# Optimization experiments

Hardware: AMD Instinct MI355X
Metric: run time of the kernel (lower is better)

Reference implementation:

```python
import jax, jax.numpy as jnp
import numpy as np

TYPE_N = 5
EPS = 1e-6  # torch F.pairwise_distance default eps, added to the difference before the norm


def setup_inputs() -> dict:
    key = jax.random.key(0)
    k1, k2 = jax.random.split(key)
    N, D = 200000, 256
    x = jax.random.normal(k1, (N, D), dtype=jnp.float32)
    y_real = jax.random.normal(k2, (N, TYPE_N), dtype=jnp.float32)
    return {"x": x, "y_real": y_real}


def reference(x, y_real):
    xf = x.reshape(x.shape[0], -1)                      # [N, D]
    labels = jnp.argmax(y_real, axis=1)                 # [N]
    dt = xf.dtype

    # per-class counts and centroid sums (segment reduce, one pass)
    counts = jax.ops.segment_sum(jnp.ones((xf.shape[0],), dt), labels, num_segments=TYPE_N)  # [C]
    sums = jax.ops.segment_sum(xf, labels, num_segments=TYPE_N)                              # [C, D]
    safe_counts = jnp.maximum(counts, 1.0)
    center = jnp.where(counts[:, None] > 0, sums / safe_counts[:, None], 0.0)                # [C, D]

    # positive loss: mean intra-class distance to centroid, summed over present classes
    d = jnp.linalg.norm(xf - center[labels] + EPS, axis=1)                                   # [N]
    per_class_mean = jax.ops.segment_sum(d, labels, num_segments=TYPE_N) / safe_counts       # [C]
    present = (counts > 0) & (jnp.sum(center, axis=1) != 0)                                  # [C]
    loss_pos = jnp.sum(jnp.where(present, per_class_mean, 0.0))
    real_n = jnp.sum(present.astype(dt))

    # negative loss: mean pairwise distance between present centers (C is tiny)
    diff = center[:, None, :] - center[None, :, :] + EPS                                     # [C, C, D]
    pd = jnp.linalg.norm(diff, axis=-1)                                                      # [C, C]
    triu = jnp.triu(jnp.ones((TYPE_N, TYPE_N), bool), k=1)
    pair_mask = triu & present[:, None] & present[None, :]
    n_pairs = real_n * (real_n - 1.0) / 2.0
    loss_neg = jnp.where(real_n > 1,
                         jnp.sum(jnp.where(pair_mask, pd, 0.0)) / jnp.maximum(n_pairs, 1.0),
                         0.0)

    loss_pos = jnp.where(real_n > 0, loss_pos / jnp.maximum(real_n, 1.0), 1.0)
    return loss_pos / (loss_neg + loss_pos)
```

## Files before the change

### kernel.cpp

```cpp
#include <hip/hip_runtime.h>
#include <math.h>

#define TYPE_N 5
#define D 256
#define EPS 1e-6f
#define NCOPY 16
#define RPB 100

#define OFF_CNTP   (NCOPY * TYPE_N * D)
#define OFF_CENTER (OFF_CNTP + NCOPY * TYPE_N)
#define OFF_CNTF   (OFF_CENTER + TYPE_N * D)
#define OFF_DSUM   (OFF_CNTF + TYPE_N)
#define OFF_CME    (OFF_DSUM + NCOPY * TYPE_N)
#define WS_FLOATS  (OFF_CME + TYPE_N * D)

__device__ __forceinline__ int argmax5(const float* __restrict__ yr) {
    int lab = 0;
    float best = yr[0];
    #pragma unroll
    for (int c = 1; c < TYPE_N; ++c) {
        float v = yr[c];
        if (v > best) { best = v; lab = c; }
    }
    return lab;
}

__global__ __launch_bounds__(256) void k1_sums(const float* __restrict__ x,
                                               const float* __restrict__ y,
                                               float* __restrict__ ws, int N) {
    __shared__ float lsum[4][TYPE_N][D];
    __shared__ float lcnt[4][TYPE_N];
    const int lane = threadIdx.x & 63;
    const int sub  = threadIdx.x >> 6;
    const int r0   = blockIdx.x * RPB;
    const int rows = (N - r0 < RPB) ? (N - r0) : RPB;

    float acc[TYPE_N][4] = {};
    float cnt[TYPE_N] = {};
    const float cw = (lane == 0) ? 1.0f : 0.0f;

    const int ng = rows >> 2;
    for (int i = 0; i < ng; ++i) {
        const int rb = r0 + i * 4;
        const int lab0 = argmax5(y + (size_t)rb * TYPE_N);
        const int lab1 = argmax5(y + (size_t)(rb + 1) * TYPE_N);
        const int lab2 = argmax5(y + (size_t)(rb + 2) * TYPE_N);
        const int lab3 = argmax5(y + (size_t)(rb + 3) * TYPE_N);
        int lab = lab0;
        lab = (sub == 1) ? lab1 : lab;
        lab = (sub == 2) ? lab2 : lab;
        lab = (sub == 3) ? lab3 : lab;
        const float4 v = *reinterpret_cast<const float4*>(
            x + (size_t)(rb + sub) * D + lane * 4);
        #pragma unroll
        for (int c = 0; c < TYPE_N; ++c) {
            const float m = (lab == c) ? 1.0f : 0.0f;
            acc[c][0] = fmaf(m, v.x, acc[c][0]);
            acc[c][1] = fmaf(m, v.y, acc[c][1]);
            acc[c][2] = fmaf(m, v.z, acc[c][2]);
            acc[c][3] = fmaf(m, v.w, acc[c][3]);
            cnt[c]    = fmaf(m, cw, cnt[c]);
        }
    }
    for (int r = r0 + (ng << 2) + sub; r < r0 + rows; r += 4) {
        const int lab = argmax5(y + (size_t)r * TYPE_N);
        const float4 v = *reinterpret_cast<const float4*>(
            x + (size_t)r * D + lane * 4);
        #pragma unroll
        for (int c = 0; c < TYPE_N; ++c) {
            const float m = (lab == c) ? 1.0f : 0.0f;
            acc[c][0] = fmaf(m, v.x, acc[c][0]);
            acc[c][1] = fmaf(m, v.y, acc[c][1]);
            acc[c][2] = fmaf(m, v.z, acc[c][2]);
            acc[c][3] = fmaf(m, v.w, acc[c][3]);
            cnt[c]    = fmaf(m, cw, cnt[c]);
        }
    }

    #pragma unroll
    for (int c = 0; c < TYPE_N; ++c) {
        *reinterpret_cast<float4*>(&lsum[sub][c][lane * 4]) =
            make_float4(acc[c][0], acc[c][1], acc[c][2], acc[c][3]);
        if (lane == 0) lcnt[sub][c] = cnt[c];
    }
    __syncthreads();
    const int t = threadIdx.x;
    float* sums = ws + (size_t)(blockIdx.x % NCOPY) * (TYPE_N * D);
    #pragma unroll
    for (int c = 0; c < TYPE_N; ++c) {
        float s = lsum[0][c][t] + lsum[1][c][t] + lsum[2][c][t] + lsum[3][c][t];
        atomicAdd(&sums[c * D + t], s);
    }
    if (t < TYPE_N) {
        float s = lcnt[0][t] + lcnt[1][t] + lcnt[2][t] + lcnt[3][t];
        atomicAdd(&ws[OFF_CNTP + (blockIdx.x % NCOPY) * TYPE_N + t], s);
    }
}

__global__ __launch_bounds__(256) void k2_center(float* __restrict__ ws) {
    const int t = threadIdx.x;
    float cnts[TYPE_N];
    #pragma unroll
    for (int c = 0; c < TYPE_N; ++c) {
        float s = 0.f;
        #pragma unroll
        for (int p = 0; p < NCOPY; ++p) s += ws[OFF_CNTP + p * TYPE_N + c];
        cnts[c] = s;
    }
    float* center = ws + OFF_CENTER;
    float* cme    = ws + OFF_CME;
    #pragma unroll
    for (int c = 0; c < TYPE_N; ++c) {
        float s = 0.f;
        #pragma unroll
        for (int p = 0; p < NCOPY; ++p) s += ws[p * TYPE_N * D + c * D + t];
        float sc = fmaxf(cnts[c], 1.0f);
        float ctr = (cnts[c] > 0.f) ? s / sc : 0.f;
        center[c * D + t] = ctr;
        cme[c * D + t]    = ctr - EPS;
    }
    if (t < TYPE_N) ws[OFF_CNTF + t] = cnts[t];
}

__global__ __launch_bounds__(256) void k3_dist(const float* __restrict__ x,
                                               const float* __restrict__ y,
                                               float* __restrict__ ws, int N) {
    __shared__ float lds[4][TYPE_N];
    const int lane = threadIdx.x & 63;
    const int wid  = threadIdx.x >> 6;
    const int r = blockIdx.x * 256 + threadIdx.x;

    int lab = 0;
    float d = 0.f;
    if (r < N) {
        lab = argmax5(y + (size_t)r * TYPE_N);
        const float4* xr = reinterpret_cast<const float4*>(x + (size_t)r * D);
        const float4* cr = reinterpret_cast<const float4*>(ws + OFF_CME + lab * D);
        float ss[4] = {0.f, 0.f, 0.f, 0.f};
        #pragma unroll 8
        for (int i = 0; i < 64; ++i) {
            const float4 a = xr[i];
            const float4 b = cr[i];
            const float t0 = a.x - b.x;
            const float t1 = a.y - b.y;
            const float t2 = a.z - b.z;
            const float t3 = a.w - b.w;
            float s = fmaf(t0, t0, t1 * t1);
            s = fmaf(t2, t2, s);
            s = fmaf(t3, t3, s);
            ss[i & 3] += s;
        }
        d = sqrtf(ss[0] + ss[1] + ss[2] + ss[3]);
    }

    #pragma unroll
    for (int c = 0; c < TYPE_N; ++c) {
        float v = (lab == c) ? d : 0.f;
        #pragma unroll
        for (int off = 32; off > 0; off >>= 1) v += __shfl_xor(v, off);
        if (lane == 0) lds[wid][c] = v;
    }
    __syncthreads();
    if (threadIdx.x < TYPE_N) {
        float s = lds[0][threadIdx.x] + lds[1][threadIdx.x] +
                  lds[2][threadIdx.x] + lds[3][threadIdx.x];
        atomicAdd(&ws[OFF_DSUM + (blockIdx.x % NCOPY) * TYPE_N + threadIdx.x], s);
    }
}

__global__ __launch_bounds__(64) void k4_final(const float* __restrict__ ws,
                                               float* __restrict__ out) {
    const int lane = threadIdx.x;
    const float* center = ws + OFF_CENTER;
    const float* counts = ws + OFF_CNTF;
    const float* dsp    = ws + OFF_DSUM;

    float csum[TYPE_N];
    #pragma unroll
    for (int c = 0; c < TYPE_N; ++c) {
        float s = 0.f;
        #pragma unroll
        for (int k = 0; k < 4; ++k) s += center[c * D + lane * 4 + k];
        #pragma unroll
        for (int off = 32; off > 0; off >>= 1) s += __shfl_xor(s, off);
        csum[c] = s;
    }

    float cnts[TYPE_N], dsum[TYPE_N];
    bool present[TYPE_N];
    float real_n = 0.f;
    #pragma unroll
    for (int c = 0; c < TYPE_N; ++c) {
        cnts[c] = counts[c];
        float s = 0.f;
        #pragma unroll
        for (int p = 0; p < NCOPY; ++p) s += dsp[p * TYPE_N + c];
        dsum[c] = s;
        present[c] = (cnts[c] > 0.f) && (csum[c] != 0.f);
        real_n += present[c] ? 1.f : 0.f;
    }

    float loss_pos = 0.f;
    #pragma unroll
    for (int c = 0; c < TYPE_N; ++c) {
        float pcm = dsum[c] / fmaxf(cnts[c], 1.f);
        loss_pos += present[c] ? pcm : 0.f;
    }
    loss_pos = (real_n > 0.f) ? loss_pos / fmaxf(real_n, 1.f) : 1.0f;

    float pairsum = 0.f;
    #pragma unroll
    for (int i = 0; i < TYPE_N; ++i) {
        #pragma unroll
        for (int j = i + 1; j < TYPE_N; ++j) {
            float s = 0.f;
            #pragma unroll
            for (int k = 0; k < 4; ++k) {
                float dd = center[i * D + lane * 4 + k] - center[j * D + lane * 4 + k] + EPS;
                s += dd * dd;
            }
            #pragma unroll
            for (int off = 32; off > 0; off >>= 1) s += __shfl_xor(s, off);
            float pd = sqrtf(s);
            pairsum += (present[i] && present[j]) ? pd : 0.f;
        }
    }
    float n_pairs = real_n * (real_n - 1.f) * 0.5f;
    float loss_neg = (real_n > 1.f) ? pairsum / fmaxf(n_pairs, 1.f) : 0.f;

    if (lane == 0) out[0] = loss_pos / (loss_neg + loss_pos);
}

extern "C" void kernel_launch(void* const* d_in, const int* in_sizes, int n_in,
                              void* d_out, int out_size, void* d_ws, size_t ws_size,
                              hipStream_t stream) {
    const float* x = (const float*)d_in[0];
    const float* y = (const float*)d_in[1];
    float* out = (float*)d_out;
    float* ws  = (float*)d_ws;
    const int N = in_sizes[0] / D;

    (void)hipMemsetAsync(d_ws, 0, (size_t)WS_FLOATS * sizeof(float), stream);

    const int grid1 = (N + RPB - 1) / RPB;
    k1_sums<<<grid1, 256, 0, stream>>>(x, y, ws, N);
    k2_center<<<1, 256, 0, stream>>>(ws);
    const int grid3 = (N + 255) / 256;
    k3_dist<<<grid3, 256, 0, stream>>>(x, y, ws, N);
    k4_final<<<1, 64, 0, stream>>>(ws, out);
}
```

Before: 115.2 us.

## Give each wave a contiguous 32-row slice with four loads in flight

Changes the k1_sums row mapping so each wave owns a contiguous chunk of 32 rows instead of interleaving one row per wave out of each group of four. Each iteration now issues four independent float4 loads per lane, which raises memory-level parallelism. Rows per block go from 100 to 128, so the grid has fewer blocks and fewer atomic flushes. The cost is more live registers and more FMAs per iteration, plus a smaller grid that may leave some CUs less busy.

```diff
diff --git a/kernel.cpp b/kernel.cpp
--- a/kernel.cpp
+++ b/kernel.cpp
@@ -5,7 +5,7 @@
 #define D 256
 #define EPS 1e-6f
 #define NCOPY 16
-#define RPB 100
+#define RPB 128
 
 #define OFF_CNTP   (NCOPY * TYPE_N * D)
 #define OFF_CENTER (OFF_CNTP + NCOPY * TYPE_N)
@@ -34,35 +34,58 @@
     const int sub  = threadIdx.x >> 6;
     const int r0   = blockIdx.x * RPB;
     const int rows = (N - r0 < RPB) ? (N - r0) : RPB;
+    const int wbase = r0 + 32 * sub;
+    int wrows = rows - 32 * sub;
+    wrows = (wrows < 0) ? 0 : ((wrows > 32) ? 32 : wrows);
 
     float acc[TYPE_N][4] = {};
     float cnt[TYPE_N] = {};
     const float cw = (lane == 0) ? 1.0f : 0.0f;
 
-    const int ng = rows >> 2;
+    const int ng = wrows >> 2;
     for (int i = 0; i < ng; ++i) {
-        const int rb = r0 + i * 4;
-        const int lab0 = argmax5(y + (size_t)rb * TYPE_N);
+        const int rb = wbase + i * 4;
+        const int lab0 = argmax5(y + (size_t)(rb + 0) * TYPE_N);
         const int lab1 = argmax5(y + (size_t)(rb + 1) * TYPE_N);
         const int lab2 = argmax5(y + (size_t)(rb + 2) * TYPE_N);
         const int lab3 = argmax5(y + (size_t)(rb + 3) * TYPE_N);
-        int lab = lab0;
-        lab = (sub == 1) ? lab1 : lab;
-        lab = (sub == 2) ? lab2 : lab;
-        lab = (sub == 3) ? lab3 : lab;
-        const float4 v = *reinterpret_cast<const float4*>(
-            x + (size_t)(rb + sub) * D + lane * 4);
+        const float4 v0 = *reinterpret_cast<const float4*>(
+            x + (size_t)(rb + 0) * D + lane * 4);
+        const float4 v1 = *reinterpret_cast<const float4*>(
+            x + (size_t)(rb + 1) * D + lane * 4);
+        const float4 v2 = *reinterpret_cast<const float4*>(
+            x + (size_t)(rb + 2) * D + lane * 4);
+        const float4 v3 = *reinterpret_cast<const float4*>(
+            x + (size_t)(rb + 3) * D + lane * 4);
         #pragma unroll
         for (int c = 0; c < TYPE_N; ++c) {
-            const float m = (lab == c) ? 1.0f : 0.0f;
-            acc[c][0] = fmaf(m, v.x, acc[c][0]);
-            acc[c][1] = fmaf(m, v.y, acc[c][1]);
-            acc[c][2] = fmaf(m, v.z, acc[c][2]);
-            acc[c][3] = fmaf(m, v.w, acc[c][3]);
-            cnt[c]    = fmaf(m, cw, cnt[c]);
-        }
-    }
-    for (int r = r0 + (ng << 2) + sub; r < r0 + rows; r += 4) {
+            const float m0 = (lab0 == c) ? 1.0f : 0.0f;
+            acc[c][0] = fmaf(m0, v0.x, acc[c][0]);
+            acc[c][1] = fmaf(m0, v0.y, acc[c][1]);
+            acc[c][2] = fmaf(m0, v0.z, acc[c][2]);
+            acc[c][3] = fmaf(m0, v0.w, acc[c][3]);
+            cnt[c]    = fmaf(m0, cw, cnt[c]);
+            const float m1 = (lab1 == c) ? 1.0f : 0.0f;
+            acc[c][0] = fmaf(m1, v1.x, acc[c][0]);
+            acc[c][1] = fmaf(m1, v1.y, acc[c][1]);
+            acc[c][2] = fmaf(m1, v1.z, acc[c][2]);
+            acc[c][3] = fmaf(m1, v1.w, acc[c][3]);
+            cnt[c]    = fmaf(m1, cw, cnt[c]);
+            const float m2 = (lab2 == c) ? 1.0f : 0.0f;
+            acc[c][0] = fmaf(m2, v2.x, acc[c][0]);
+            acc[c][1] = fmaf(m2, v2.y, acc[c][1]);
+            acc[c][2] = fmaf(m2, v2.z, acc[c][2]);
+            acc[c][3] = fmaf(m2, v2.w, acc[c][3]);
+            cnt[c]    = fmaf(m2, cw, cnt[c]);
+            const float m3 = (lab3 == c) ? 1.0f : 0.0f;
+            acc[c][0] = fmaf(m3, v3.x, acc[c][0]);
+            acc[c][1] = fmaf(m3, v3.y, acc[c][1]);
+            acc[c][2] = fmaf(m3, v3.z, acc[c][2]);
+            acc[c][3] = fmaf(m3, v3.w, acc[c][3]);
+            cnt[c]    = fmaf(m3, cw, cnt[c]);
+        }
+    }
+    for (int r = wbase + (ng << 2); r < wbase + wrows; ++r) {
         const int lab = argmax5(y + (size_t)r * TYPE_N);
         const float4 v = *reinterpret_cast<const float4*>(
             x + (size_t)r * D + lane * 4);
```

After: 109.7 us, median of 2. 1.05x faster.
